# Optimization experiments

Measured on AMD Instinct MI355X. Metric: run time of the kernel, lower is better.

## Reference

```python
import jax, jax.numpy as jnp
import numpy as np

H, W = 128, 128
FOCAL_X = FOCAL_Y = 128.0
NEAR = 0.3
N_GAUSS = 2048
EPS = 1e-4  # regularizer on 2D covariance diagonal


def q2r(q):
    """Quaternion (w,x,y,z) [N,4] -> rotation matrices [N,3,3]."""
    q = q / jnp.linalg.norm(q, axis=-1, keepdims=True)
    w, x, y, z = q[:, 0], q[:, 1], q[:, 2], q[:, 3]
    R = jnp.stack([
        1 - 2 * (y * y + z * z), 2 * (x * y - w * z), 2 * (x * z + w * y),
        2 * (x * y + w * z), 1 - 2 * (x * x + z * z), 2 * (y * z - w * x),
        2 * (x * z - w * y), 2 * (y * z + w * x), 1 - 2 * (x * x + y * y),
    ], axis=-1).reshape(-1, 3, 3)
    return R


def setup_inputs():
    key = jax.random.key(0)
    ks = jax.random.split(key, 6)
    # gaussians placed inside the camera frustum (camera looks along +z)
    xy = jax.random.uniform(ks[0], (N_GAUSS, 2), minval=-1.5, maxval=1.5)
    z = jax.random.uniform(ks[1], (N_GAUSS, 1), minval=2.0, maxval=6.0)
    pos = jnp.concatenate([xy * z / 4.0, z], axis=-1)
    rgb = jax.random.normal(ks[2], (N_GAUSS, 3))
    opa = jax.random.normal(ks[3], (N_GAUSS,))
    quat = jax.random.normal(ks[4], (N_GAUSS, 4))
    scale = jax.random.uniform(ks[5], (N_GAUSS, 3), minval=0.01, maxval=0.05)
    ang = 0.05  # small camera rotation about y
    rot = jnp.array([[np.cos(ang), 0.0, np.sin(ang)],
                     [0.0, 1.0, 0.0],
                     [-np.sin(ang), 0.0, np.cos(ang)]], dtype=jnp.float32)
    tran = jnp.array([0.0, 0.0, 0.1], dtype=jnp.float32)
    return {"pos": pos, "rgb": rgb, "opa": opa, "quat": quat,
            "scale": scale, "rot": rot, "tran": tran}


def _forward(pos, rgb, opa, quat, scale, rot, tran):
    # ---- project: world -> camera -> image space (Gaussian3ds.project) ----
    pos_cam = pos @ rot.T + tran                       # [N,3]
    x, y, z = pos_cam[:, 0], pos_cam[:, 1], pos_cam[:, 2]
    r = jnp.linalg.norm(pos_cam, axis=-1)              # depth = ||p_cam||
    u, v = x / z, y / z                                # normalized image coords
    zero = jnp.zeros_like(z)
    # jacobian of (x/z, y/z, ||p||) wrt camera coords (jacobian_torch)
    J = jnp.stack([1.0 / z, zero, -x / (z * z),
                   zero, 1.0 / z, -y / (z * z),
                   x / r, y / r, z / r], axis=-1).reshape(-1, 3, 3)
    # 3D covariance: R S S^T R^T with abs scale activation
    Rm = q2r(quat)
    s = jnp.abs(scale) + 1e-4
    RS = Rm * s[:, None, :]                            # R @ diag(s)
    cov3d = jnp.einsum('nij,nkj->nik', RS, RS)
    JW = jnp.einsum('nij,jk->nik', J, rot)
    cov2d = jnp.einsum('nij,njk,nlk->nil', JW, cov3d, JW)[:, :2, :2]
    a = cov2d[:, 0, 0] + EPS
    b = cov2d[:, 0, 1]
    c = cov2d[:, 1, 1] + EPS
    det = a * c - b * b
    ia, ib, ic = c / det, -b / det, a / det            # inverse 2x2 cov entries
    rgb_s = jax.nn.sigmoid(rgb)
    opa_s = jax.nn.sigmoid(opa)
    # ---- global front-to-back depth sort ----
    order = jnp.argsort(r)
    u, v = u[order], v[order]
    ia, ib, ic = ia[order], ib[order], ic[order]
    opa_s, zs = opa_s[order], z[order]
    rgb_s = rgb_s[order]
    # ---- alpha composite over all pixels (tiles merged -> dense) ----
    px = (jnp.arange(W) - W / 2 + 0.5) / FOCAL_X
    py = (jnp.arange(H) - H / 2 + 0.5) / FOCAL_Y
    yy, xx = jnp.meshgrid(py, px, indexing='ij')
    pxf, pyf = xx.reshape(-1), yy.reshape(-1)          # [P]
    dx = pxf[:, None] - u[None, :]                     # [P,N]
    dy = pyf[:, None] - v[None, :]
    power = -0.5 * (ia * dx * dx + 2.0 * ib * dx * dy + ic * dy * dy)
    alpha = jnp.clip(opa_s * jnp.exp(power), 0.0, 0.99)
    alpha = alpha * (zs > NEAR)                        # near-plane cull as mask
    T = jnp.cumprod(1.0 - alpha, axis=1)
    T_excl = jnp.concatenate([jnp.ones((T.shape[0], 1), T.dtype), T[:, :-1]], axis=1)
    img = (T_excl * alpha) @ rgb_s                     # [P,3]
    return img.reshape(H, W, 3)


def reference(pos, rgb, opa, quat, scale, rot, tran):
    return _forward(pos, rgb, opa, quat, scale, rot, tran)
```

## Files before the change

kernel.cpp:

```cpp
#include <hip/hip_runtime.h>
#include <hip/hip_bf16.h>

#define NG     2048
#define HW     128
#define NPIX   (HW*HW)
#define SEG    16
#define CHUNK  (NG/SEG)
#define NEARZ  0.3f
#define GEPS   1e-4f
#define LOG2E  1.4426950408889634f

__device__ float  g_r[NG];
__device__ float4 g_ga_u[NG];
__device__ float4 g_gb_u[NG];
__device__ float  g_cb_u[NG];
__device__ float4 g_ga_s[NG];
__device__ float4 g_gb_s[NG];
__device__ float  g_cb_s[NG];

__device__ __forceinline__ float sigm(float x) { return 1.0f / (1.0f + __expf(-x)); }

__device__ __forceinline__ bool detect_f32(const void* rot) {
    return ((const unsigned short*)rot)[1] != 0;
}
__device__ __forceinline__ float ld(const void* p, int idx, bool f32) {
    if (f32) return ((const float*)p)[idx];
    return __bfloat162float(((const __hip_bfloat16*)p)[idx]);
}

__global__ __launch_bounds__(256)
void preprocess_kernel(const void* __restrict__ pos,
                       const void* __restrict__ rgb,
                       const void* __restrict__ opa,
                       const void* __restrict__ quat,
                       const void* __restrict__ scale,
                       const void* __restrict__ rot,
                       const void* __restrict__ tran)
{
    int i = blockIdx.x * blockDim.x + threadIdx.x;
    if (i >= NG) return;
    bool f32 = detect_f32(rot);

    float R[9], T3[3];
    #pragma unroll
    for (int k = 0; k < 9; k++) R[k] = ld(rot, k, f32);
    #pragma unroll
    for (int k = 0; k < 3; k++) T3[k] = ld(tran, k, f32);

    float p0 = ld(pos, i*3+0, f32), p1 = ld(pos, i*3+1, f32), p2 = ld(pos, i*3+2, f32);
    float x = R[0]*p0 + R[1]*p1 + R[2]*p2 + T3[0];
    float y = R[3]*p0 + R[4]*p1 + R[5]*p2 + T3[1];
    float z = R[6]*p0 + R[7]*p1 + R[8]*p2 + T3[2];
    float r = sqrtf(x*x + y*y + z*z);
    float iz = 1.0f / z;
    float u = x * iz, v = y * iz;

    float qw = ld(quat, i*4+0, f32), qx = ld(quat, i*4+1, f32);
    float qy = ld(quat, i*4+2, f32), qz = ld(quat, i*4+3, f32);
    float qn = 1.0f / sqrtf(qw*qw + qx*qx + qy*qy + qz*qz);
    qw *= qn; qx *= qn; qy *= qn; qz *= qn;
    float Rm[3][3];
    Rm[0][0] = 1.0f - 2.0f*(qy*qy + qz*qz);
    Rm[0][1] = 2.0f*(qx*qy - qw*qz);
    Rm[0][2] = 2.0f*(qx*qz + qw*qy);
    Rm[1][0] = 2.0f*(qx*qy + qw*qz);
    Rm[1][1] = 1.0f - 2.0f*(qx*qx + qz*qz);
    Rm[1][2] = 2.0f*(qy*qz - qw*qx);
    Rm[2][0] = 2.0f*(qx*qz - qw*qy);
    Rm[2][1] = 2.0f*(qy*qz + qw*qx);
    Rm[2][2] = 1.0f - 2.0f*(qx*qx + qy*qy);

    float s[3];
    #pragma unroll
    for (int k = 0; k < 3; k++) s[k] = fabsf(ld(scale, i*3+k, f32)) + 1e-4f;

    float RS[3][3];
    #pragma unroll
    for (int a = 0; a < 3; a++)
        #pragma unroll
        for (int b = 0; b < 3; b++) RS[a][b] = Rm[a][b] * s[b];
    float C3[3][3];
    #pragma unroll
    for (int a = 0; a < 3; a++)
        #pragma unroll
        for (int b = 0; b < 3; b++)
            C3[a][b] = RS[a][0]*RS[b][0] + RS[a][1]*RS[b][1] + RS[a][2]*RS[b][2];

    float nx = -x * iz * iz, ny = -y * iz * iz;
    float jw0[3], jw1[3];
    #pragma unroll
    for (int k = 0; k < 3; k++) {
        jw0[k] = iz * R[0*3+k] + nx * R[2*3+k];
        jw1[k] = iz * R[1*3+k] + ny * R[2*3+k];
    }
    float t0[3], t1[3];
    #pragma unroll
    for (int j = 0; j < 3; j++) {
        t0[j] = C3[j][0]*jw0[0] + C3[j][1]*jw0[1] + C3[j][2]*jw0[2];
        t1[j] = C3[j][0]*jw1[0] + C3[j][1]*jw1[1] + C3[j][2]*jw1[2];
    }
    float a = jw0[0]*t0[0] + jw0[1]*t0[1] + jw0[2]*t0[2] + GEPS;
    float b = jw0[0]*t1[0] + jw0[1]*t1[1] + jw0[2]*t1[2];
    float c = jw1[0]*t1[0] + jw1[1]*t1[1] + jw1[2]*t1[2] + GEPS;
    float idet = 1.0f / (a*c - b*b);
    float Af = -0.5f * LOG2E * (c * idet);
    float Bf = -LOG2E * (-b * idet);
    float Cf = -0.5f * LOG2E * (a * idet);

    float om = (z > NEARZ) ? sigm(ld(opa, i, f32)) : 0.0f;
    float cr = sigm(ld(rgb, i*3+0, f32));
    float cg = sigm(ld(rgb, i*3+1, f32));
    float cb = sigm(ld(rgb, i*3+2, f32));

    g_r[i]    = r;
    g_ga_u[i] = make_float4(u, v, Af, Bf);
    g_gb_u[i] = make_float4(Cf, om, cr, cg);
    g_cb_u[i] = cb;
}

__global__ __launch_bounds__(256)
void sort_kernel()
{
    __shared__ float rs[NG];
    int tid = threadIdx.x;
    for (int k = tid; k < NG; k += 256) rs[k] = g_r[k];
    __syncthreads();

    int g      = (blockIdx.x * 256 + tid) >> 4;
    int lane16 = tid & 15;
    float ri = rs[g];

    int rank = 0;
    int jbase = lane16 * (NG / 16);
    #pragma unroll 4
    for (int jj = 0; jj < NG / 16; jj++) {
        int j = jbase + ((jj + 2 * lane16) & (NG / 16 - 1));
        float rj = rs[j];
        rank += (rj < ri) || (rj == ri && j < g);
    }
    #pragma unroll
    for (int d = 1; d < 16; d <<= 1) rank += __shfl_xor(rank, d);

    if (lane16 == 0) {
        g_ga_s[rank] = g_ga_u[g];
        g_gb_s[rank] = g_gb_u[g];
        g_cb_s[rank] = g_cb_u[g];
    }
}

__global__ __launch_bounds__(1024)
void raster_kernel(void* __restrict__ out, const void* __restrict__ rot)
{
    __shared__ float4 comb[SEG * 64];

    int tid  = threadIdx.x;
    int lane = tid & 63;
    int w    = __builtin_amdgcn_readfirstlane(tid >> 6);

    int pix = blockIdx.x * 64 + lane;
    int row = pix >> 7;
    int col = pix & 127;
    float pxf = (col - 63.5f) * (1.0f / 128.0f);
    float pyf = (row - 63.5f) * (1.0f / 128.0f);

    float T = 1.0f, Cr = 0.0f, Cg = 0.0f, Cb = 0.0f;
    int base = w * CHUNK;
    #pragma unroll 4
    for (int k = 0; k < CHUNK; k++) {
        float4 a4 = g_ga_s[base + k];
        float4 b4 = g_gb_s[base + k];
        float  cb = g_cb_s[base + k];
        float dx = pxf - a4.x;
        float dy = pyf - a4.y;
        float p  = (a4.z * dx + a4.w * dy) * dx;
        p = fmaf(b4.x * dy, dy, p);
        p = fminf(p, 0.0f);
        float alpha = fminf(b4.y * __builtin_amdgcn_exp2f(p), 0.99f);
        float wgt = T * alpha;
        Cr = fmaf(wgt, b4.z, Cr);
        Cg = fmaf(wgt, b4.w, Cg);
        Cb = fmaf(wgt, cb, Cb);
        T *= (1.0f - alpha);
    }

    comb[w * 64 + lane] = make_float4(T, Cr, Cg, Cb);
    __syncthreads();

    if (tid < 64) {
        float Ta = 1.0f, Ra = 0.0f, Ga = 0.0f, Ba = 0.0f;
        #pragma unroll
        for (int s = 0; s < SEG; s++) {
            float4 c4 = comb[s * 64 + lane];
            Ra = fmaf(Ta, c4.y, Ra);
            Ga = fmaf(Ta, c4.z, Ga);
            Ba = fmaf(Ta, c4.w, Ba);
            Ta *= c4.x;
        }
        bool f32 = detect_f32(rot);
        if (f32) {
            float* o = (float*)out;
            o[pix*3 + 0] = Ra; o[pix*3 + 1] = Ga; o[pix*3 + 2] = Ba;
        } else {
            __hip_bfloat16* o = (__hip_bfloat16*)out;
            o[pix*3 + 0] = __float2bfloat16(Ra);
            o[pix*3 + 1] = __float2bfloat16(Ga);
            o[pix*3 + 2] = __float2bfloat16(Ba);
        }
    }
}

extern "C" void kernel_launch(void* const* d_in, const int* in_sizes, int n_in,
                              void* d_out, int out_size, void* d_ws, size_t ws_size,
                              hipStream_t stream)
{
    const void* pos   = d_in[0];
    const void* rgb   = d_in[1];
    const void* opa   = d_in[2];
    const void* quat  = d_in[3];
    const void* scale = d_in[4];
    const void* rot   = d_in[5];
    const void* tran  = d_in[6];

    preprocess_kernel<<<NG/256, 256, 0, stream>>>(pos, rgb, opa, quat, scale, rot, tran);
    sort_kernel<<<(NG*16)/256, 256, 0, stream>>>();
    raster_kernel<<<NPIX/64, 1024, 0, stream>>>(d_out, rot);
}
```

Measured before the change: 98.96 us.

## Fuse preprocess and rank-sort into one kernel, simplify raster inner loop

Result: no change. 97.19 us (-1.8%).

```diff
diff --git a/kernel.cpp b/kernel.cpp
--- a/kernel.cpp
+++ b/kernel.cpp
@@ -10,10 +10,6 @@
 #define GEPS   1e-4f
 #define LOG2E  1.4426950408889634f
 
-__device__ float  g_r[NG];
-__device__ float4 g_ga_u[NG];
-__device__ float4 g_gb_u[NG];
-__device__ float  g_cb_u[NG];
 __device__ float4 g_ga_s[NG];
 __device__ float4 g_gb_s[NG];
 __device__ float  g_cb_s[NG];
@@ -29,122 +25,124 @@
 }
 
 __global__ __launch_bounds__(256)
-void preprocess_kernel(const void* __restrict__ pos,
-                       const void* __restrict__ rgb,
-                       const void* __restrict__ opa,
-                       const void* __restrict__ quat,
-                       const void* __restrict__ scale,
-                       const void* __restrict__ rot,
-                       const void* __restrict__ tran)
-{
-    int i = blockIdx.x * blockDim.x + threadIdx.x;
-    if (i >= NG) return;
-    bool f32 = detect_f32(rot);
-
-    float R[9], T3[3];
-    #pragma unroll
-    for (int k = 0; k < 9; k++) R[k] = ld(rot, k, f32);
-    #pragma unroll
-    for (int k = 0; k < 3; k++) T3[k] = ld(tran, k, f32);
-
-    float p0 = ld(pos, i*3+0, f32), p1 = ld(pos, i*3+1, f32), p2 = ld(pos, i*3+2, f32);
-    float x = R[0]*p0 + R[1]*p1 + R[2]*p2 + T3[0];
-    float y = R[3]*p0 + R[4]*p1 + R[5]*p2 + T3[1];
-    float z = R[6]*p0 + R[7]*p1 + R[8]*p2 + T3[2];
-    float r = sqrtf(x*x + y*y + z*z);
-    float iz = 1.0f / z;
-    float u = x * iz, v = y * iz;
-
-    float qw = ld(quat, i*4+0, f32), qx = ld(quat, i*4+1, f32);
-    float qy = ld(quat, i*4+2, f32), qz = ld(quat, i*4+3, f32);
-    float qn = 1.0f / sqrtf(qw*qw + qx*qx + qy*qy + qz*qz);
-    qw *= qn; qx *= qn; qy *= qn; qz *= qn;
-    float Rm[3][3];
-    Rm[0][0] = 1.0f - 2.0f*(qy*qy + qz*qz);
-    Rm[0][1] = 2.0f*(qx*qy - qw*qz);
-    Rm[0][2] = 2.0f*(qx*qz + qw*qy);
-    Rm[1][0] = 2.0f*(qx*qy + qw*qz);
-    Rm[1][1] = 1.0f - 2.0f*(qx*qx + qz*qz);
-    Rm[1][2] = 2.0f*(qy*qz - qw*qx);
-    Rm[2][0] = 2.0f*(qx*qz - qw*qy);
-    Rm[2][1] = 2.0f*(qy*qz + qw*qx);
-    Rm[2][2] = 1.0f - 2.0f*(qx*qx + qy*qy);
-
-    float s[3];
-    #pragma unroll
-    for (int k = 0; k < 3; k++) s[k] = fabsf(ld(scale, i*3+k, f32)) + 1e-4f;
-
-    float RS[3][3];
-    #pragma unroll
-    for (int a = 0; a < 3; a++)
-        #pragma unroll
-        for (int b = 0; b < 3; b++) RS[a][b] = Rm[a][b] * s[b];
-    float C3[3][3];
-    #pragma unroll
-    for (int a = 0; a < 3; a++)
-        #pragma unroll
-        for (int b = 0; b < 3; b++)
-            C3[a][b] = RS[a][0]*RS[b][0] + RS[a][1]*RS[b][1] + RS[a][2]*RS[b][2];
-
-    float nx = -x * iz * iz, ny = -y * iz * iz;
-    float jw0[3], jw1[3];
-    #pragma unroll
-    for (int k = 0; k < 3; k++) {
-        jw0[k] = iz * R[0*3+k] + nx * R[2*3+k];
-        jw1[k] = iz * R[1*3+k] + ny * R[2*3+k];
-    }
-    float t0[3], t1[3];
-    #pragma unroll
-    for (int j = 0; j < 3; j++) {
-        t0[j] = C3[j][0]*jw0[0] + C3[j][1]*jw0[1] + C3[j][2]*jw0[2];
-        t1[j] = C3[j][0]*jw1[0] + C3[j][1]*jw1[1] + C3[j][2]*jw1[2];
-    }
-    float a = jw0[0]*t0[0] + jw0[1]*t0[1] + jw0[2]*t0[2] + GEPS;
-    float b = jw0[0]*t1[0] + jw0[1]*t1[1] + jw0[2]*t1[2];
-    float c = jw1[0]*t1[0] + jw1[1]*t1[1] + jw1[2]*t1[2] + GEPS;
-    float idet = 1.0f / (a*c - b*b);
-    float Af = -0.5f * LOG2E * (c * idet);
-    float Bf = -LOG2E * (-b * idet);
-    float Cf = -0.5f * LOG2E * (a * idet);
-
-    float om = (z > NEARZ) ? sigm(ld(opa, i, f32)) : 0.0f;
-    float cr = sigm(ld(rgb, i*3+0, f32));
-    float cg = sigm(ld(rgb, i*3+1, f32));
-    float cb = sigm(ld(rgb, i*3+2, f32));
-
-    g_r[i]    = r;
-    g_ga_u[i] = make_float4(u, v, Af, Bf);
-    g_gb_u[i] = make_float4(Cf, om, cr, cg);
-    g_cb_u[i] = cb;
-}
-
-__global__ __launch_bounds__(256)
-void sort_kernel()
+void prep_sort_kernel(const void* __restrict__ pos,
+                      const void* __restrict__ rgb,
+                      const void* __restrict__ opa,
+                      const void* __restrict__ quat,
+                      const void* __restrict__ scale,
+                      const void* __restrict__ rot,
+                      const void* __restrict__ tran)
 {
     __shared__ float rs[NG];
+    __shared__ int   srank[16];
+
     int tid = threadIdx.x;
-    for (int k = tid; k < NG; k += 256) rs[k] = g_r[k];
+    bool f32 = detect_f32(rot);
+
+    float R[9], T3[3];
+    #pragma unroll
+    for (int k = 0; k < 9; k++) R[k] = ld(rot, k, f32);
+    #pragma unroll
+    for (int k = 0; k < 3; k++) T3[k] = ld(tran, k, f32);
+
+    #pragma unroll
+    for (int k = 0; k < NG / 256; k++) {
+        int j = tid + k * 256;
+        float p0 = ld(pos, j*3+0, f32), p1 = ld(pos, j*3+1, f32), p2 = ld(pos, j*3+2, f32);
+        float x = R[0]*p0 + R[1]*p1 + R[2]*p2 + T3[0];
+        float y = R[3]*p0 + R[4]*p1 + R[5]*p2 + T3[1];
+        float z = R[6]*p0 + R[7]*p1 + R[8]*p2 + T3[2];
+        rs[j] = sqrtf(x*x + y*y + z*z);
+    }
     __syncthreads();
 
-    int g      = (blockIdx.x * 256 + tid) >> 4;
+    int g      = blockIdx.x * 16 + (tid >> 4);
     int lane16 = tid & 15;
     float ri = rs[g];
-
     int rank = 0;
-    int jbase = lane16 * (NG / 16);
+    int jbase = lane16 * CHUNK;
     #pragma unroll 4
-    for (int jj = 0; jj < NG / 16; jj++) {
-        int j = jbase + ((jj + 2 * lane16) & (NG / 16 - 1));
+    for (int jj = 0; jj < CHUNK; jj++) {
+        int j = jbase + ((jj + 2 * lane16) & (CHUNK - 1));
         float rj = rs[j];
         rank += (rj < ri) || (rj == ri && j < g);
     }
     #pragma unroll
     for (int d = 1; d < 16; d <<= 1) rank += __shfl_xor(rank, d);
-
-    if (lane16 == 0) {
-        g_ga_s[rank] = g_ga_u[g];
-        g_gb_s[rank] = g_gb_u[g];
-        g_cb_s[rank] = g_cb_u[g];
+    if (lane16 == 0) srank[tid >> 4] = rank;
+    __syncthreads();
+
+    if (tid < 16) {
+        int i = blockIdx.x * 16 + tid;
+        int rk = srank[tid];
+
+        float p0 = ld(pos, i*3+0, f32), p1 = ld(pos, i*3+1, f32), p2 = ld(pos, i*3+2, f32);
+        float x = R[0]*p0 + R[1]*p1 + R[2]*p2 + T3[0];
+        float y = R[3]*p0 + R[4]*p1 + R[5]*p2 + T3[1];
+        float z = R[6]*p0 + R[7]*p1 + R[8]*p2 + T3[2];
+        float iz = 1.0f / z;
+        float u = x * iz, v = y * iz;
+
+        float qw = ld(quat, i*4+0, f32), qx = ld(quat, i*4+1, f32);
+        float qy = ld(quat, i*4+2, f32), qz = ld(quat, i*4+3, f32);
+        float qn = 1.0f / sqrtf(qw*qw + qx*qx + qy*qy + qz*qz);
+        qw *= qn; qx *= qn; qy *= qn; qz *= qn;
+        float Rm[3][3];
+        Rm[0][0] = 1.0f - 2.0f*(qy*qy + qz*qz);
+        Rm[0][1] = 2.0f*(qx*qy - qw*qz);
+        Rm[0][2] = 2.0f*(qx*qz + qw*qy);
+        Rm[1][0] = 2.0f*(qx*qy + qw*qz);
+        Rm[1][1] = 1.0f - 2.0f*(qx*qx + qz*qz);
+        Rm[1][2] = 2.0f*(qy*qz - qw*qx);
+        Rm[2][0] = 2.0f*(qx*qz - qw*qy);
+        Rm[2][1] = 2.0f*(qy*qz + qw*qx);
+        Rm[2][2] = 1.0f - 2.0f*(qx*qx + qy*qy);
+
+        float s[3];
+        #pragma unroll
+        for (int k = 0; k < 3; k++) s[k] = fabsf(ld(scale, i*3+k, f32)) + 1e-4f;
+
+        float RS[3][3];
+        #pragma unroll
+        for (int a = 0; a < 3; a++)
+            #pragma unroll
+            for (int b = 0; b < 3; b++) RS[a][b] = Rm[a][b] * s[b];
+        float C3[3][3];
+        #pragma unroll
+        for (int a = 0; a < 3; a++)
+            #pragma unroll
+            for (int b = 0; b < 3; b++)
+                C3[a][b] = RS[a][0]*RS[b][0] + RS[a][1]*RS[b][1] + RS[a][2]*RS[b][2];
+
+        float nx = -x * iz * iz, ny = -y * iz * iz;
+        float jw0[3], jw1[3];
+        #pragma unroll
+        for (int k = 0; k < 3; k++) {
+            jw0[k] = iz * R[0*3+k] + nx * R[2*3+k];
+            jw1[k] = iz * R[1*3+k] + ny * R[2*3+k];
+        }
+        float t0[3], t1[3];
+        #pragma unroll
+        for (int j = 0; j < 3; j++) {
+            t0[j] = C3[j][0]*jw0[0] + C3[j][1]*jw0[1] + C3[j][2]*jw0[2];
+            t1[j] = C3[j][0]*jw1[0] + C3[j][1]*jw1[1] + C3[j][2]*jw1[2];
+        }
+        float a = jw0[0]*t0[0] + jw0[1]*t0[1] + jw0[2]*t0[2] + GEPS;
+        float b = jw0[0]*t1[0] + jw0[1]*t1[1] + jw0[2]*t1[2];
+        float c = jw1[0]*t1[0] + jw1[1]*t1[1] + jw1[2]*t1[2] + GEPS;
+        float idet = 1.0f / (a*c - b*b);
+        float Af = -0.5f * LOG2E * (c * idet);
+        float Bf = -LOG2E * (-b * idet);
+        float Cf = -0.5f * LOG2E * (a * idet);
+
+        float om = (z > NEARZ) ? sigm(ld(opa, i, f32)) : 0.0f;
+        float cr = sigm(ld(rgb, i*3+0, f32));
+        float cg = sigm(ld(rgb, i*3+1, f32));
+        float cb = sigm(ld(rgb, i*3+2, f32));
+
+        g_ga_s[rk] = make_float4(u, v, Af, Bf);
+        g_gb_s[rk] = make_float4(Cf, om, cr, cg);
+        g_cb_s[rk] = cb;
     }
 }
 
@@ -165,7 +163,7 @@
 
     float T = 1.0f, Cr = 0.0f, Cg = 0.0f, Cb = 0.0f;
     int base = w * CHUNK;
-    #pragma unroll 4
+    #pragma unroll 8
     for (int k = 0; k < CHUNK; k++) {
         float4 a4 = g_ga_s[base + k];
         float4 b4 = g_gb_s[base + k];
@@ -174,13 +172,12 @@
         float dy = pyf - a4.y;
         float p  = (a4.z * dx + a4.w * dy) * dx;
         p = fmaf(b4.x * dy, dy, p);
-        p = fminf(p, 0.0f);
         float alpha = fminf(b4.y * __builtin_amdgcn_exp2f(p), 0.99f);
         float wgt = T * alpha;
         Cr = fmaf(wgt, b4.z, Cr);
         Cg = fmaf(wgt, b4.w, Cg);
         Cb = fmaf(wgt, cb, Cb);
-        T *= (1.0f - alpha);
+        T -= wgt;
     }
 
     comb[w * 64 + lane] = make_float4(T, Cr, Cg, Cb);
@@ -196,8 +193,7 @@
             Ba = fmaf(Ta, c4.w, Ba);
             Ta *= c4.x;
         }
-        bool f32 = detect_f32(rot);
-        if (f32) {
+        if (detect_f32(rot)) {
             float* o = (float*)out;
             o[pix*3 + 0] = Ra; o[pix*3 + 1] = Ga; o[pix*3 + 2] = Ba;
         } else {
@@ -221,7 +217,6 @@
     const void* rot   = d_in[5];
     const void* tran  = d_in[6];
 
-    preprocess_kernel<<<NG/256, 256, 0, stream>>>(pos, rgb, opa, quat, scale, rot, tran);
-    sort_kernel<<<(NG*16)/256, 256, 0, stream>>>();
+    prep_sort_kernel<<<NG/16, 256, 0, stream>>>(pos, rgb, opa, quat, scale, rot, tran);
     raster_kernel<<<NPIX/64, 1024, 0, stream>>>(d_out, rot);
 }
```
